# Optimization experiments

Measured on AMD Instinct MI355X. Metric: run time of the kernel, lower is better.

## Reference

```python
import jax, jax.numpy as jnp
import numpy as np

N_NODES = 100000
N_PART = 5000
N_EDGES = 1000000
D_NODE = 128
D_PART = 128
D_ATT = 20


def setup_inputs() -> dict:
    key = jax.random.key(0)
    ks = jax.random.split(key, 20)
    inp = {
        "nodes_hidden": jax.random.normal(ks[0], (N_NODES, D_NODE), jnp.float32),
        "particles_hidden": jax.random.normal(ks[1], (N_PART, D_PART), jnp.float32),
        "global_rep": jax.random.normal(ks[2], (N_PART, D_NODE), jnp.float32),
        "src": jax.random.randint(ks[3], (N_EDGES,), 0, N_NODES, jnp.int32),
        "dst": jax.random.randint(ks[4], (N_EDGES,), 0, N_PART, jnp.int32),
        "key_W": jax.random.normal(ks[5], (D_NODE, D_ATT), jnp.float32) * 0.05,
        "key_b": jnp.zeros((D_ATT,), jnp.float32),
        "val_W": jax.random.normal(ks[6], (D_NODE, D_PART), jnp.float32) * 0.05,
        "val_b": jnp.zeros((D_PART,), jnp.float32),
        "q_W": jax.random.normal(ks[7], (D_PART + D_NODE, D_ATT), jnp.float32) * 0.05,
        "q_b": jnp.zeros((D_ATT,), jnp.float32),
        "W_ih": jax.random.normal(ks[8], (3 * D_PART, D_PART), jnp.float32) * 0.05,
        "W_hh": jax.random.normal(ks[9], (3 * D_PART, D_PART), jnp.float32) * 0.05,
        "b_ih": jnp.zeros((3 * D_PART,), jnp.float32),
        "b_hh": jnp.zeros((3 * D_PART,), jnp.float32),
        "ln_g": jnp.ones((D_PART,), jnp.float32),
        "ln_b": jnp.zeros((D_PART,), jnp.float32),
        "mlp_W1": jax.random.normal(ks[10], (D_PART, 64), jnp.float32) * 0.05,
        "mlp_b1": jnp.zeros((64,), jnp.float32),
        "mlp_W2": jax.random.normal(ks[11], (64, D_PART), jnp.float32) * 0.05,
        "mlp_b2": jnp.zeros((D_PART,), jnp.float32),
    }
    return inp


def reference(nodes_hidden, particles_hidden, global_rep, src, dst,
              key_W, key_b, val_W, val_b, q_W, q_b,
              W_ih, W_hh, b_ih, b_hh, ln_g, ln_b,
              mlp_W1, mlp_b1, mlp_W2, mlp_b2):
    norm = jnp.float32(1.0) / jnp.sqrt(jnp.float32(D_ATT))
    keys = nodes_hidden @ key_W + key_b          # [N, 20]
    vals = nodes_hidden @ val_W + val_b          # [N, P]
    q_in = jnp.concatenate([particles_hidden, global_rep], axis=1)
    query = q_in @ q_W + q_b                     # [Np, 20]

    # per-edge raw attention (ReLU'd copy in edges.data is unused downstream)
    att = jnp.sum(keys[src] * query[dst], axis=1) * norm     # [E]
    msg = att[:, None] * vals[src]                            # [E, P]
    weighted_sum = jax.ops.segment_sum(msg, dst, num_segments=particles_hidden.shape[0])

    # GRUCell(input=weighted_sum, hidden=particles_hidden), torch semantics
    gi = weighted_sum @ W_ih.T + b_ih
    gh = particles_hidden @ W_hh.T + b_hh
    i_r, i_z, i_n = jnp.split(gi, 3, axis=1)
    h_r, h_z, h_n = jnp.split(gh, 3, axis=1)
    r = jax.nn.sigmoid(i_r + h_r)
    z = jax.nn.sigmoid(i_z + h_z)
    n = jnp.tanh(i_n + r * h_n)
    h_new = (1.0 - z) * n + z * particles_hidden

    # LayerNorm (eps=1e-5)
    mu = jnp.mean(h_new, axis=-1, keepdims=True)
    var = jnp.mean(jnp.square(h_new - mu), axis=-1, keepdims=True)
    ln = (h_new - mu) * jax.lax.rsqrt(var + 1e-5) * ln_g + ln_b

    mlp_out = jax.nn.relu(ln @ mlp_W1 + mlp_b1) @ mlp_W2 + mlp_b2
    return particles_hidden + mlp_out
```

## Files before the change

### kernel.cpp

```cpp
#include <hip/hip_runtime.h>
#include <math.h>

#define N_NODES 100000
#define N_PART  5000
#define N_EDGES 1000000
#define D_NODE  128
#define D_PART  128
#define D_ATT   20
#define NBLK    128
#define EPB     ((N_EDGES + NBLK - 1) / NBLK)
#define TPV6    8
#define QBLKS   (N_PART / TPV6)
#define CVTBLKS 1024

__device__ __forceinline__ float sigmoid_(float x) { return 1.f / (1.f + __expf(-x)); }
__device__ __forceinline__ float tanh_(float x)    { return 1.f - 2.f / (__expf(2.f * x) + 1.f); }

__device__ __forceinline__ float4 bf4_to_f4(uint2 r) {
    float4 f;
    f.x = __uint_as_float(r.x << 16);
    f.y = __uint_as_float(r.x & 0xFFFF0000u);
    f.z = __uint_as_float(r.y << 16);
    f.w = __uint_as_float(r.y & 0xFFFF0000u);
    return f;
}

__device__ __forceinline__ unsigned short f_to_bf(float v) {
    uint32_t u = __float_as_uint(v);
    return (unsigned short)((u + 0x7FFFu + ((u >> 16) & 1u)) >> 16);
}

__device__ __forceinline__ void gru_body(float4 acc[4],
    float4 w0, float4 w1, float4 w2, float4 w3,
    float4 x0, float4 x1, float4 x2, float4 x3)
{
    acc[0].x += x0.x * w0.x + x0.y * w1.x + x0.z * w2.x + x0.w * w3.x;
    acc[0].y += x0.x * w0.y + x0.y * w1.y + x0.z * w2.y + x0.w * w3.y;
    acc[0].z += x0.x * w0.z + x0.y * w1.z + x0.z * w2.z + x0.w * w3.z;
    acc[0].w += x0.x * w0.w + x0.y * w1.w + x0.z * w2.w + x0.w * w3.w;
    acc[1].x += x1.x * w0.x + x1.y * w1.x + x1.z * w2.x + x1.w * w3.x;
    acc[1].y += x1.x * w0.y + x1.y * w1.y + x1.z * w2.y + x1.w * w3.y;
    acc[1].z += x1.x * w0.z + x1.y * w1.z + x1.z * w2.z + x1.w * w3.z;
    acc[1].w += x1.x * w0.w + x1.y * w1.w + x1.z * w2.w + x1.w * w3.w;
    acc[2].x += x2.x * w0.x + x2.y * w1.x + x2.z * w2.x + x2.w * w3.x;
    acc[2].y += x2.x * w0.y + x2.y * w1.y + x2.z * w2.y + x2.w * w3.y;
    acc[2].z += x2.x * w0.z + x2.y * w1.z + x2.z * w2.z + x2.w * w3.z;
    acc[2].w += x2.x * w0.w + x2.y * w1.w + x2.z * w2.w + x2.w * w3.w;
    acc[3].x += x3.x * w0.x + x3.y * w1.x + x3.z * w2.x + x3.w * w3.x;
    acc[3].y += x3.x * w0.y + x3.y * w1.y + x3.z * w2.y + x3.w * w3.y;
    acc[3].z += x3.x * w0.z + x3.y * w1.z + x3.z * w2.z + x3.w * w3.z;
    acc[3].w += x3.x * w0.w + x3.y * w1.w + x3.z * w2.w + x3.w * w3.w;
}

__device__ __forceinline__ size_t wpk_idx(int k, int jn) {
    return ((size_t)(k >> 1) * 128 + (jn >> 2)) * 8 + ((k & 1) << 2) + (jn & 3);
}

__global__ __launch_bounds__(256) void fused_front_kernel(
    const float* __restrict__ valW, const float* __restrict__ Wih,
    const float* __restrict__ Whh, unsigned short* __restrict__ Wpack,
    const float* __restrict__ valb, float* __restrict__ bvec,
    const int* __restrict__ dst, int* __restrict__ blockhist,
    const float* __restrict__ ph, const float* __restrict__ gr,
    const float* __restrict__ qW, const float* __restrict__ qb,
    const float* __restrict__ keyW, const float* __restrict__ keyb,
    float* __restrict__ qk, float* __restrict__ qoff,
    const float* __restrict__ nodes, unsigned short* __restrict__ nodes_bf)
{
    __shared__ float pool[5000];
    int blk = blockIdx.x;
    int t = threadIdx.x;

    if (blk < 12) {
        float (*sA)[33] = (float (*)[33])pool;
        float (*sB)[33] = (float (*)[33])(pool + 2112);
        int bk = blk / 6, bj = blk - bk * 6;
        int k0 = bk * 64, j0 = bj * 64;
        int tk = t >> 4, tj = t & 15;
        float acc[4][4];
        #pragma unroll
        for (int i = 0; i < 4; i++)
            #pragma unroll
            for (int j = 0; j < 4; j++) acc[i][j] = 0.f;

        for (int mc = 0; mc < 128; mc += 32) {
            #pragma unroll
            for (int s = 0; s < 2; s++) {
                int f = t + s * 256;
                int r = f >> 3, c4 = (f & 7) * 4;
                *(float4*)&sA[r][c4] = *(const float4*)(valW + (size_t)(k0 + r) * 128 + mc + c4);
                *(float4*)&sB[r][c4] = *(const float4*)(Wih  + (size_t)(j0 + r) * 128 + mc + c4);
            }
            __syncthreads();
            #pragma unroll 8
            for (int mm = 0; mm < 32; mm++) {
                float a0 = sA[tk * 4 + 0][mm], a1 = sA[tk * 4 + 1][mm];
                float a2 = sA[tk * 4 + 2][mm], a3 = sA[tk * 4 + 3][mm];
                float b0 = sB[tj * 4 + 0][mm], b1 = sB[tj * 4 + 1][mm];
                float b2 = sB[tj * 4 + 2][mm], b3 = sB[tj * 4 + 3][mm];
                acc[0][0] += a0 * b0; acc[0][1] += a0 * b1; acc[0][2] += a0 * b2; acc[0][3] += a0 * b3;
                acc[1][0] += a1 * b0; acc[1][1] += a1 * b1; acc[1][2] += a1 * b2; acc[1][3] += a1 * b3;
                acc[2][0] += a2 * b0; acc[2][1] += a2 * b1; acc[2][2] += a2 * b2; acc[2][3] += a2 * b3;
                acc[3][0] += a3 * b0; acc[3][1] += a3 * b1; acc[3][2] += a3 * b2; acc[3][3] += a3 * b3;
            }
            __syncthreads();
        }
        #pragma unroll
        for (int i = 0; i < 4; i++) {
            int k = k0 + tk * 4 + i;
            #pragma unroll
            for (int j = 0; j < 4; j++) {
                int oj = j0 + tj * 4 + j;
                int jn = (oj & 127) * 4 + (oj >> 7);
                Wpack[wpk_idx(k, jn)] = f_to_bf(acc[i][j]);
            }
        }
    } else if (blk < 14) {
        for (int f = t; f < 8192; f += 256) {
            int e = (blk - 12) * 8192 + f;
            int k = e >> 7, c = e & 127;
            Wpack[wpk_idx(k, c * 4 + 3)] = 0;
        }
    } else if (blk < 142) {
        #pragma unroll
        for (int s = 0; s < 2; s++) {
            int idx = 65536 + (blk - 14) * 512 + s * 256 + t;
            int k = idx >> 9;
            int jn = idx & 511;
            int j = (jn & 3) * 128 + (jn >> 2);
            int kp = k - 128;
            float v = 0.f;
            if (j < 256)       v = Whh[j * 128 + kp];
            else if (j >= 384) v = Whh[(j - 128) * 128 + kp];
            Wpack[wpk_idx(k, jn)] = f_to_bf(v);
        }
    } else if (blk < 144) {
        int c = (blk - 142) * 256 + t;
        if (c < 384) {
            float acc = 0.f;
            #pragma unroll 8
            for (int m = 0; m < 128; m++) acc += valb[m] * Wih[c * 128 + m];
            bvec[c] = acc;
        }
    } else if (blk < 272) {
        int b = blk - 144;
        int* h = (int*)pool;
        for (int i = t; i < N_PART; i += 256) h[i] = 0;
        __syncthreads();
        int beg = b * EPB, end = min(beg + EPB, N_EDGES);
        for (int e = beg + t; e < end; e += 256)
            atomicAdd(&h[dst[e]], 1);
        __syncthreads();
        for (int i = t; i < N_PART; i += 256)
            blockhist[(size_t)b * N_PART + i] = h[i];
    } else if (blk < 897) {
        float (*s_in)[260] = (float (*)[260])pool;
        float (*s_q)[20]   = (float (*)[20])(pool + 2080);
        float (*s_kw)[21]  = (float (*)[21])(pool + 2240);
        float* s_kb = pool + 4928;
        float* s_qb = pool + 4948;

        int pbase = (blk - 272) * TPV6;

        for (int f = t; f < TPV6 * 64; f += 256) {
            int pl = f >> 6, r = f & 63;
            int c4 = r * 4;
            int p = pbase + pl;
            float4 v;
            if (c4 < 128) v = *(const float4*)(ph + (size_t)p * 128 + c4);
            else          v = *(const float4*)(gr + (size_t)p * 128 + (c4 - 128));
            *(float4*)&s_in[pl][c4] = v;
        }
        for (int f = t; f < 2560; f += 256) {
            int j = f / 20, a = f - j * 20;
            s_kw[j][a] = keyW[f];
        }
        if (t < 20) { s_kb[t] = keyb[t]; s_qb[t] = qb[t]; }
        __syncthreads();

        if (t < 160) {
            int pl = t / 20, a = t - (t / 20) * 20;
            float acc = s_qb[a];
            const float* qwp = qW + a;
            #pragma unroll 8
            for (int k = 0; k < 256; k++) acc += s_in[pl][k] * qwp[k * 20];
            s_q[pl][a] = acc;
        }
        __syncthreads();

        {
            int pl = t >> 5, j0 = (t & 31) * 4;
            float acc0 = 0.f, acc1 = 0.f, acc2 = 0.f, acc3 = 0.f;
            #pragma unroll
            for (int a = 0; a < 20; a++) {
                float qv = s_q[pl][a];
                acc0 += qv * s_kw[j0][a];
                acc1 += qv * s_kw[j0 + 1][a];
                acc2 += qv * s_kw[j0 + 2][a];
                acc3 += qv * s_kw[j0 + 3][a];
            }
            float4 o; o.x = acc0; o.y = acc1; o.z = acc2; o.w = acc3;
            *(float4*)(qk + (size_t)(pbase + pl) * 128 + j0) = o;

            if (t < TPV6) {
                float acc = 0.f;
                #pragma unroll
                for (int a = 0; a < 20; a++) acc += s_kb[a] * s_q[t][a];
                qoff[pbase + t] = acc;
            }
        }
    } else {
        const uint64_t total8 = (uint64_t)N_NODES * 128 / 8;
        uint64_t cb = (uint64_t)(blk - 897) * 256 + t;
        const uint32_t* inb = (const uint32_t*)nodes;
        uint32_t* outb = (uint32_t*)nodes_bf;
        for (uint64_t c = cb; c < total8; c += (uint64_t)CVTBLKS * 256) {
            uint4 a = *(const uint4*)(inb + c * 8);
            uint4 b = *(const uint4*)(inb + c * 8 + 4);
            uint32_t r0 = (a.x + 0x7FFFu + ((a.x >> 16) & 1u)) >> 16;
            uint32_t r1 = (a.y + 0x7FFFu + ((a.y >> 16) & 1u)) >> 16;
            uint32_t r2 = (a.z + 0x7FFFu + ((a.z >> 16) & 1u)) >> 16;
            uint32_t r3 = (a.w + 0x7FFFu + ((a.w >> 16) & 1u)) >> 16;
            uint32_t r4 = (b.x + 0x7FFFu + ((b.x >> 16) & 1u)) >> 16;
            uint32_t r5 = (b.y + 0x7FFFu + ((b.y >> 16) & 1u)) >> 16;
            uint32_t r6 = (b.z + 0x7FFFu + ((b.z >> 16) & 1u)) >> 16;
            uint32_t r7 = (b.w + 0x7FFFu + ((b.w >> 16) & 1u)) >> 16;
            uint4 o;
            o.x = r0 | (r1 << 16);
            o.y = r2 | (r3 << 16);
            o.z = r4 | (r5 << 16);
            o.w = r6 | (r7 << 16);
            *(uint4*)(outb + c * 4) = o;
        }
    }
}

__global__ __launch_bounds__(256) void colscan_kernel(
    int* __restrict__ blockhist, int* __restrict__ totals)
{
    int i = blockIdx.x * 256 + threadIdx.x;
    if (i >= N_PART) return;
    int run = 0;
    for (int b = 0; b < NBLK; b++) {
        size_t idx = (size_t)b * N_PART + i;
        int v = blockhist[idx];
        blockhist[idx] = run;
        run += v;
    }
    totals[i] = run;
}

__global__ __launch_bounds__(256) void scan_kernel(
    const int* __restrict__ totals, int* __restrict__ offsets)
{
    __shared__ int ss[256];
    int t = threadIdx.x;
    const int CH = 20;
    int beg = t * CH;
    int end = min(beg + CH, N_PART);
    int lsum = 0;
    for (int i = beg; i < end; i++) lsum += totals[i];
    ss[t] = lsum;
    __syncthreads();
    for (int off = 1; off < 256; off <<= 1) {
        int v = (t >= off) ? ss[t - off] : 0;
        __syncthreads();
        ss[t] += v;
        __syncthreads();
    }
    int base = ss[t] - lsum;
    for (int i = beg; i < end; i++) {
        offsets[i] = base;
        base += totals[i];
    }
    if (t == 0) offsets[N_PART] = N_EDGES;
}

__global__ __launch_bounds__(256) void scatter_sorted_kernel(
    const int* __restrict__ src, const int* __restrict__ dst,
    const int* __restrict__ offsets, const int* __restrict__ blockhist,
    int* __restrict__ ssrc)
{
    __shared__ int cur[N_PART];
    int b = blockIdx.x;
    for (int i = threadIdx.x; i < N_PART; i += 256)
        cur[i] = offsets[i] + blockhist[(size_t)b * N_PART + i];
    __syncthreads();
    int beg = b * EPB, end = min(beg + EPB, N_EDGES);
    for (int e = beg + threadIdx.x; e < end; e += 256) {
        int d = dst[e];
        int pos = atomicAdd(&cur[d], 1);
        ssrc[pos] = src[e];
    }
}

__global__ __launch_bounds__(256) void edge_agg_bf16_kernel(
    const unsigned short* __restrict__ nodes_bf, const float* __restrict__ qk,
    const float* __restrict__ qoff,
    const int* __restrict__ offsets, const int* __restrict__ ssrc,
    float* __restrict__ agg, float* __restrict__ att_sum)
{
    const float norm = 0.22360679774997896f;
    int p = blockIdx.x;
    int tid = threadIdx.x;
    int lane = tid & 63;
    int wave = tid >> 6;
    int half = lane >> 5;
    int colq = (lane & 31) * 4;

    const float4 q = *(const float4*)(qk + (size_t)p * 128 + colq);
    float qo = qoff[p];
    int beg = offsets[p], end = offsets[p + 1];
    int n = end - beg;
    int np = (n + 1) >> 1;
    int npfull = n >> 1;

    float4 a = {0.f, 0.f, 0.f, 0.f};
    float asum = 0.f;

    int pi = wave;
    for (; pi + 12 < npfull; pi += 16) {
        int e0 = beg + 2 * pi + half;
        int s0 = ssrc[e0];
        int s1 = ssrc[e0 + 8];
        int s2 = ssrc[e0 + 16];
        int s3 = ssrc[e0 + 24];
        uint2 r0 = *(const uint2*)(nodes_bf + (size_t)s0 * 128 + colq);
        uint2 r1 = *(const uint2*)(nodes_bf + (size_t)s1 * 128 + colq);
        uint2 r2 = *(const uint2*)(nodes_bf + (size_t)s2 * 128 + colq);
        uint2 r3 = *(const uint2*)(nodes_bf + (size_t)s3 * 128 + colq);
        float4 x0 = bf4_to_f4(r0);
        float4 x1 = bf4_to_f4(r1);
        float4 x2 = bf4_to_f4(r2);
        float4 x3 = bf4_to_f4(r3);
        float d0 = x0.x * q.x + x0.y * q.y + x0.z * q.z + x0.w * q.w;
        float d1 = x1.x * q.x + x1.y * q.y + x1.z * q.z + x1.w * q.w;
        float d2 = x2.x * q.x + x2.y * q.y + x2.z * q.z + x2.w * q.w;
        float d3 = x3.x * q.x + x3.y * q.y + x3.z * q.z + x3.w * q.w;
        #pragma unroll
        for (int off = 1; off <= 16; off <<= 1) {
            d0 += __shfl_xor(d0, off, 64);
            d1 += __shfl_xor(d1, off, 64);
            d2 += __shfl_xor(d2, off, 64);
            d3 += __shfl_xor(d3, off, 64);
        }
        float t0 = (d0 + qo) * norm;
        float t1 = (d1 + qo) * norm;
        float t2 = (d2 + qo) * norm;
        float t3 = (d3 + qo) * norm;
        a.x += t0 * x0.x + t1 * x1.x + t2 * x2.x + t3 * x3.x;
        a.y += t0 * x0.y + t1 * x1.y + t2 * x2.y + t3 * x3.y;
        a.z += t0 * x0.z + t1 * x1.z + t2 * x2.z + t3 * x3.z;
        a.w += t0 * x0.w + t1 * x1.w + t2 * x2.w + t3 * x3.w;
        asum += t0 + t1 + t2 + t3;
    }
    for (; pi < np; pi += 4) {
        int e0 = beg + 2 * pi;
        bool has1 = (e0 + 1 < end);
        int s0 = ssrc[e0];
        int s1 = has1 ? ssrc[e0 + 1] : s0;
        int s = half ? s1 : s0;
        uint2 r = *(const uint2*)(nodes_bf + (size_t)s * 128 + colq);
        float4 x = bf4_to_f4(r);
        float d = x.x * q.x + x.y * q.y + x.z * q.z + x.w * q.w;
        #pragma unroll
        for (int off = 1; off <= 16; off <<= 1) d += __shfl_xor(d, off, 64);
        float att = (d + qo) * norm;
        if (half && !has1) att = 0.f;
        a.x += att * x.x; a.y += att * x.y; a.z += att * x.z; a.w += att * x.w;
        asum += att;
    }

    a.x += __shfl_xor(a.x, 32, 64);
    a.y += __shfl_xor(a.y, 32, 64);
    a.z += __shfl_xor(a.z, 32, 64);
    a.w += __shfl_xor(a.w, 32, 64);
    asum += __shfl_xor(asum, 32, 64);

    __shared__ float s_acc[4][128];
    __shared__ float s_as[4];
    if (lane < 32) {
        *(float4*)&s_acc[wave][colq] = a;
        if (lane == 0) s_as[wave] = asum;
    }
    __syncthreads();

    if (tid < 128) {
        float v = s_acc[0][tid] + s_acc[1][tid] + s_acc[2][tid] + s_acc[3][tid];
        agg[(size_t)p * 128 + tid] = v;
        if (tid == 0) att_sum[p] = s_as[0] + s_as[1] + s_as[2] + s_as[3];
    }
}

__global__ __launch_bounds__(256) void gru_fused_v8(
    const float* __restrict__ agg, const float* __restrict__ att_sum,
    const float* __restrict__ ph,
    const unsigned short* __restrict__ Wpack, const float* __restrict__ bvec,
    const float* __restrict__ bih, const float* __restrict__ bhh,
    const float* __restrict__ lng, const float* __restrict__ lnb,
    const float* __restrict__ W1, const float* __restrict__ b1,
    const float* __restrict__ W2, const float* __restrict__ b2,
    float* __restrict__ out)
{
    __shared__ float s_in[TPV6][256];
    __shared__ float s_ln[TPV6][128];
    __shared__ float s_hid[TPV6][64];

    int t = threadIdx.x;
    int pbase = blockIdx.x * TPV6;

    for (int f = t; f < TPV6 * 64; f += 256) {
        int pl = f >> 6, r = f & 63;
        int c4 = r * 4;
        int p = pbase + pl;
        float4 v;
        if (c4 < 128) v = *(const float4*)(agg + (size_t)p * 128 + c4);
        else          v = *(const float4*)(ph + (size_t)p * 128 + (c4 - 128));
        *(float4*)&s_in[pl][c4] = v;
    }

    int c  = t & 127;
    int pg = t >> 7;
    float4 cb, bv;
    cb.x = bih[c]       + bhh[c];        bv.x = bvec[c];
    cb.y = bih[128 + c] + bhh[128 + c];  bv.y = bvec[128 + c];
    cb.z = bih[256 + c];                 bv.z = bvec[256 + c];
    cb.w = bhh[256 + c];                 bv.w = 0.f;
    float4 acc[4];
    #pragma unroll
    for (int i = 0; i < 4; i++) {
        float as = att_sum[pbase + pg * 4 + i];
        acc[i].x = cb.x + as * bv.x;
        acc[i].y = cb.y + as * bv.y;
        acc[i].z = cb.z + as * bv.z;
        acc[i].w = cb.w + as * bv.w;
    }
    __syncthreads();

    const uint4* wpk = (const uint4*)Wpack;
    uint4 wu = wpk[c];
    uint4 wv = wpk[128 + c];
    float4 x0 = *(const float4*)&s_in[pg * 4 + 0][0];
    float4 x1 = *(const float4*)&s_in[pg * 4 + 1][0];
    float4 x2 = *(const float4*)&s_in[pg * 4 + 2][0];
    float4 x3 = *(const float4*)&s_in[pg * 4 + 3][0];
    for (int k = 0; k < 256; k += 4) {
        uint4 cu = wu, cv = wv;
        float4 cx0 = x0, cx1 = x1, cx2 = x2, cx3 = x3;
        if (k < 252) {
            int k2n = (k >> 1) + 2;
            wu = wpk[(size_t)k2n * 128 + c];
            wv = wpk[(size_t)(k2n + 1) * 128 + c];
            x0 = *(const float4*)&s_in[pg * 4 + 0][k + 4];
            x1 = *(const float4*)&s_in[pg * 4 + 1][k + 4];
            x2 = *(const float4*)&s_in[pg * 4 + 2][k + 4];
            x3 = *(const float4*)&s_in[pg * 4 + 3][k + 4];
        }
        float4 w0 = bf4_to_f4(make_uint2(cu.x, cu.y));
        float4 w1 = bf4_to_f4(make_uint2(cu.z, cu.w));
        float4 w2 = bf4_to_f4(make_uint2(cv.x, cv.y));
        float4 w3 = bf4_to_f4(make_uint2(cv.z, cv.w));
        gru_body(acc, w0, w1, w2, w3, cx0, cx1, cx2, cx3);
    }

    #pragma unroll
    for (int i = 0; i < 4; i++) {
        int pl = pg * 4 + i;
        float r = sigmoid_(acc[i].x);
        float z = sigmoid_(acc[i].y);
        float n = tanh_(acc[i].z + r * acc[i].w);
        float h = s_in[pl][128 + c];
        s_ln[pl][c] = (1.f - z) * n + z * h;
    }
    __syncthreads();

    {
        int wv2 = t >> 6, l = t & 63;
        for (int pl = wv2; pl < TPV6; pl += 4) {
            float v0 = s_ln[pl][l * 2], v1 = s_ln[pl][l * 2 + 1];
            float sum = v0 + v1, sq = v0 * v0 + v1 * v1;
            #pragma unroll
            for (int off = 1; off <= 32; off <<= 1) {
                sum += __shfl_xor(sum, off, 64);
                sq  += __shfl_xor(sq, off, 64);
            }
            float mu = sum * (1.f / 128.f);
            float var = sq * (1.f / 128.f) - mu * mu;
            float rstd = rsqrtf(var + 1e-5f);
            s_ln[pl][l * 2]     = (v0 - mu) * rstd * lng[l * 2] + lnb[l * 2];
            s_ln[pl][l * 2 + 1] = (v1 - mu) * rstd * lng[l * 2 + 1] + lnb[l * 2 + 1];
        }
    }
    __syncthreads();

    for (int idx = t; idx < TPV6 * 64; idx += 256) {
        int pl = idx >> 6, u = idx & 63;
        float a0 = b1[u];
        #pragma unroll 4
        for (int k = 0; k < 128; k++) a0 += s_ln[pl][k] * W1[k * 64 + u];
        s_hid[pl][u] = fmaxf(a0, 0.f);
    }
    __syncthreads();

    for (int idx = t; idx < TPV6 * 32; idx += 256) {
        int pl = idx >> 5, qd = idx & 31;
        int c4 = qd * 4;
        float4 o = *(const float4*)(b2 + c4);
        #pragma unroll 4
        for (int u = 0; u < 64; u++) {
            float av = s_hid[pl][u];
            float4 w = *(const float4*)(W2 + u * 128 + c4);
            o.x += av * w.x; o.y += av * w.y; o.z += av * w.z; o.w += av * w.w;
        }
        float4 h4 = *(const float4*)&s_in[pl][128 + c4];
        float4 res;
        res.x = h4.x + o.x; res.y = h4.y + o.y;
        res.z = h4.z + o.z; res.w = h4.w + o.w;
        *(float4*)(out + (size_t)(pbase + pl) * 128 + c4) = res;
    }
}

extern "C" void kernel_launch(void* const* d_in, const int* in_sizes, int n_in,
                              void* d_out, int out_size, void* d_ws, size_t ws_size,
                              hipStream_t stream) {
    const float* nodes = (const float*)d_in[0];
    const float* ph    = (const float*)d_in[1];
    const float* gr    = (const float*)d_in[2];
    const int*   src   = (const int*)d_in[3];
    const int*   dst   = (const int*)d_in[4];
    const float* keyW  = (const float*)d_in[5];
    const float* keyb  = (const float*)d_in[6];
    const float* valW  = (const float*)d_in[7];
    const float* valb  = (const float*)d_in[8];
    const float* qW    = (const float*)d_in[9];
    const float* qb    = (const float*)d_in[10];
    const float* Wih   = (const float*)d_in[11];
    const float* Whh   = (const float*)d_in[12];
    const float* bih   = (const float*)d_in[13];
    const float* bhh   = (const float*)d_in[14];
    const float* lng   = (const float*)d_in[15];
    const float* lnb   = (const float*)d_in[16];
    const float* W1    = (const float*)d_in[17];
    const float* b1    = (const float*)d_in[18];
    const float* W2    = (const float*)d_in[19];
    const float* b2    = (const float*)d_in[20];
    float* out = (float*)d_out;

    float* ws_f      = (float*)d_ws;
    float* qk        = ws_f;
    float* qoff      = qk + 640000;
    float* agg       = qoff + 5008;
    float* att_sum   = agg + 640000;
    int*   totals    = (int*)(att_sum + 5008);
    int*   offsets   = totals + 5008;
    int*   blockhist = offsets + 5008;
    int*   ssrc      = blockhist + (size_t)NBLK * N_PART;
    unsigned short* Wpack = (unsigned short*)(ssrc + 1000000);
    float* bvec      = (float*)(Wpack + 131072);
    unsigned short* nodes_bf = (unsigned short*)(bvec + 512);

    fused_front_kernel<<<897 + CVTBLKS, 256, 0, stream>>>(
        valW, Wih, Whh, Wpack,
        valb, bvec,
        dst, blockhist,
        ph, gr, qW, qb, keyW, keyb, qk, qoff,
        nodes, nodes_bf);

    colscan_kernel<<<(N_PART + 255) / 256, 256, 0, stream>>>(blockhist, totals);

    scan_kernel<<<1, 256, 0, stream>>>(totals, offsets);

    scatter_sorted_kernel<<<NBLK, 256, 0, stream>>>(src, dst, offsets, blockhist, ssrc);

    edge_agg_bf16_kernel<<<N_PART, 256, 0, stream>>>(nodes_bf, qk, qoff, offsets, ssrc, agg, att_sum);

    gru_fused_v8<<<N_PART / TPV6, 256, 0, stream>>>(
        agg, att_sum, ph, Wpack, bvec, bih, bhh, lng, lnb, W1, b1, W2, b2, out);
}
```

Measured before the change: 269.3 us.

## Use fp32 packed GRU weights and halve particles per block in GRU kernel

The combined GRU weight matrix is now stored as plain fp32 in a simple row-major [k][512] layout instead of a bf16 pair-interleaved pack, so the GRU kernel loads float4s directly with no conversion. The GRU kernel also processes 4 particles per block instead of 8, which doubles the grid to 1250 blocks and halves per-thread accumulators. The goal is more parallelism and less register pressure in this tail kernel. In exchange, weight traffic per block doubles in bytes and the total weight reads across blocks grow, and precision of the GRU weights goes up slightly.

```diff
diff --git a/kernel.cpp b/kernel.cpp
--- a/kernel.cpp
+++ b/kernel.cpp
@@ -11,6 +11,7 @@
 #define EPB     ((N_EDGES + NBLK - 1) / NBLK)
 #define TPV6    8
 #define QBLKS   (N_PART / TPV6)
+#define TPV9    4
 #define CVTBLKS 1024
 
 __device__ __forceinline__ float sigmoid_(float x) { return 1.f / (1.f + __expf(-x)); }
@@ -25,14 +26,9 @@
     return f;
 }
 
-__device__ __forceinline__ unsigned short f_to_bf(float v) {
-    uint32_t u = __float_as_uint(v);
-    return (unsigned short)((u + 0x7FFFu + ((u >> 16) & 1u)) >> 16);
-}
-
-__device__ __forceinline__ void gru_body(float4 acc[4],
+__device__ __forceinline__ void gru_body2(float4 acc[2],
     float4 w0, float4 w1, float4 w2, float4 w3,
-    float4 x0, float4 x1, float4 x2, float4 x3)
+    float4 x0, float4 x1)
 {
     acc[0].x += x0.x * w0.x + x0.y * w1.x + x0.z * w2.x + x0.w * w3.x;
     acc[0].y += x0.x * w0.y + x0.y * w1.y + x0.z * w2.y + x0.w * w3.y;
@@ -42,23 +38,11 @@
     acc[1].y += x1.x * w0.y + x1.y * w1.y + x1.z * w2.y + x1.w * w3.y;
     acc[1].z += x1.x * w0.z + x1.y * w1.z + x1.z * w2.z + x1.w * w3.z;
     acc[1].w += x1.x * w0.w + x1.y * w1.w + x1.z * w2.w + x1.w * w3.w;
-    acc[2].x += x2.x * w0.x + x2.y * w1.x + x2.z * w2.x + x2.w * w3.x;
-    acc[2].y += x2.x * w0.y + x2.y * w1.y + x2.z * w2.y + x2.w * w3.y;
-    acc[2].z += x2.x * w0.z + x2.y * w1.z + x2.z * w2.z + x2.w * w3.z;
-    acc[2].w += x2.x * w0.w + x2.y * w1.w + x2.z * w2.w + x2.w * w3.w;
-    acc[3].x += x3.x * w0.x + x3.y * w1.x + x3.z * w2.x + x3.w * w3.x;
-    acc[3].y += x3.x * w0.y + x3.y * w1.y + x3.z * w2.y + x3.w * w3.y;
-    acc[3].z += x3.x * w0.z + x3.y * w1.z + x3.z * w2.z + x3.w * w3.z;
-    acc[3].w += x3.x * w0.w + x3.y * w1.w + x3.z * w2.w + x3.w * w3.w;
-}
-
-__device__ __forceinline__ size_t wpk_idx(int k, int jn) {
-    return ((size_t)(k >> 1) * 128 + (jn >> 2)) * 8 + ((k & 1) << 2) + (jn & 3);
 }
 
 __global__ __launch_bounds__(256) void fused_front_kernel(
     const float* __restrict__ valW, const float* __restrict__ Wih,
-    const float* __restrict__ Whh, unsigned short* __restrict__ Wpack,
+    const float* __restrict__ Whh, float* __restrict__ Wbig,
     const float* __restrict__ valb, float* __restrict__ bvec,
     const int* __restrict__ dst, int* __restrict__ blockhist,
     const float* __restrict__ ph, const float* __restrict__ gr,
@@ -111,15 +95,14 @@
             #pragma unroll
             for (int j = 0; j < 4; j++) {
                 int oj = j0 + tj * 4 + j;
-                int jn = (oj & 127) * 4 + (oj >> 7);
-                Wpack[wpk_idx(k, jn)] = f_to_bf(acc[i][j]);
+                Wbig[(size_t)k * 512 + (oj & 127) * 4 + (oj >> 7)] = acc[i][j];
             }
         }
     } else if (blk < 14) {
         for (int f = t; f < 8192; f += 256) {
             int e = (blk - 12) * 8192 + f;
             int k = e >> 7, c = e & 127;
-            Wpack[wpk_idx(k, c * 4 + 3)] = 0;
+            Wbig[(size_t)k * 512 + c * 4 + 3] = 0.f;
         }
     } else if (blk < 142) {
         #pragma unroll
@@ -132,7 +115,7 @@
             float v = 0.f;
             if (j < 256)       v = Whh[j * 128 + kp];
             else if (j >= 384) v = Whh[(j - 128) * 128 + kp];
-            Wpack[wpk_idx(k, jn)] = f_to_bf(v);
+            Wbig[(size_t)k * 512 + jn] = v;
         }
     } else if (blk < 144) {
         int c = (blk - 142) * 256 + t;
@@ -392,24 +375,25 @@
     }
 }
 
-__global__ __launch_bounds__(256) void gru_fused_v8(
+__global__ __launch_bounds__(256) void gru_fused_v9(
     const float* __restrict__ agg, const float* __restrict__ att_sum,
     const float* __restrict__ ph,
-    const unsigned short* __restrict__ Wpack, const float* __restrict__ bvec,
+    const float* __restrict__ Wbig, const float* __restrict__ bvec,
     const float* __restrict__ bih, const float* __restrict__ bhh,
     const float* __restrict__ lng, const float* __restrict__ lnb,
     const float* __restrict__ W1, const float* __restrict__ b1,
     const float* __restrict__ W2, const float* __restrict__ b2,
     float* __restrict__ out)
 {
-    __shared__ float s_in[TPV6][256];
-    __shared__ float s_ln[TPV6][128];
-    __shared__ float s_hid[TPV6][64];
+    __shared__ float s_in[TPV9][256];
+    __shared__ float s_ln[TPV9][128];
+    __shared__ float s_hid[TPV9][64];
 
     int t = threadIdx.x;
-    int pbase = blockIdx.x * TPV6;
-
-    for (int f = t; f < TPV6 * 64; f += 256) {
+    int pbase = blockIdx.x * TPV9;
+
+    {
+        int f = t;
         int pl = f >> 6, r = f & 63;
         int c4 = r * 4;
         int p = pbase + pl;
@@ -420,16 +404,17 @@
     }
 
     int c  = t & 127;
+    int j4 = c * 4;
     int pg = t >> 7;
     float4 cb, bv;
     cb.x = bih[c]       + bhh[c];        bv.x = bvec[c];
     cb.y = bih[128 + c] + bhh[128 + c];  bv.y = bvec[128 + c];
     cb.z = bih[256 + c];                 bv.z = bvec[256 + c];
     cb.w = bhh[256 + c];                 bv.w = 0.f;
-    float4 acc[4];
+    float4 acc[2];
     #pragma unroll
-    for (int i = 0; i < 4; i++) {
-        float as = att_sum[pbase + pg * 4 + i];
+    for (int i = 0; i < 2; i++) {
+        float as = att_sum[pbase + pg * 2 + i];
         acc[i].x = cb.x + as * bv.x;
         acc[i].y = cb.y + as * bv.y;
         acc[i].z = cb.z + as * bv.z;
@@ -437,35 +422,31 @@
     }
     __syncthreads();
 
-    const uint4* wpk = (const uint4*)Wpack;
-    uint4 wu = wpk[c];
-    uint4 wv = wpk[128 + c];
-    float4 x0 = *(const float4*)&s_in[pg * 4 + 0][0];
-    float4 x1 = *(const float4*)&s_in[pg * 4 + 1][0];
-    float4 x2 = *(const float4*)&s_in[pg * 4 + 2][0];
-    float4 x3 = *(const float4*)&s_in[pg * 4 + 3][0];
+    const float* wp = Wbig + j4;
+    float4 w0 = *(const float4*)(wp);
+    float4 w1 = *(const float4*)(wp + 512);
+    float4 w2 = *(const float4*)(wp + 1024);
+    float4 w3 = *(const float4*)(wp + 1536);
+    float4 x0 = *(const float4*)&s_in[pg * 2 + 0][0];
+    float4 x1 = *(const float4*)&s_in[pg * 2 + 1][0];
     for (int k = 0; k < 256; k += 4) {
-        uint4 cu = wu, cv = wv;
-        float4 cx0 = x0, cx1 = x1, cx2 = x2, cx3 = x3;
+        float4 cw0 = w0, cw1 = w1, cw2 = w2, cw3 = w3;
+        float4 cx0 = x0, cx1 = x1;
         if (k < 252) {
-            int k2n = (k >> 1) + 2;
-            wu = wpk[(size_t)k2n * 128 + c];
-            wv = wpk[(size_t)(k2n + 1) * 128 + c];
-            x0 = *(const float4*)&s_in[pg * 4 + 0][k + 4];
-            x1 = *(const float4*)&s_in[pg * 4 + 1][k + 4];
-            x2 = *(const float4*)&s_in[pg * 4 + 2][k + 4];
-            x3 = *(const float4*)&s_in[pg * 4 + 3][k + 4];
-        }
-        float4 w0 = bf4_to_f4(make_uint2(cu.x, cu.y));
-        float4 w1 = bf4_to_f4(make_uint2(cu.z, cu.w));
-        float4 w2 = bf4_to_f4(make_uint2(cv.x, cv.y));
-        float4 w3 = bf4_to_f4(make_uint2(cv.z, cv.w));
-        gru_body(acc, w0, w1, w2, w3, cx0, cx1, cx2, cx3);
+            const float* wn = wp + (size_t)(k + 4) * 512;
+            w0 = *(const float4*)(wn);
+            w1 = *(const float4*)(wn + 512);
+            w2 = *(const float4*)(wn + 1024);
+            w3 = *(const float4*)(wn + 1536);
+            x0 = *(const float4*)&s_in[pg * 2 + 0][k + 4];
+            x1 = *(const float4*)&s_in[pg * 2 + 1][k + 4];
+        }
+        gru_body2(acc, cw0, cw1, cw2, cw3, cx0, cx1);
     }
 
     #pragma unroll
-    for (int i = 0; i < 4; i++) {
-        int pl = pg * 4 + i;
+    for (int i = 0; i < 2; i++) {
+        int pl = pg * 2 + i;
         float r = sigmoid_(acc[i].x);
         float z = sigmoid_(acc[i].y);
         float n = tanh_(acc[i].z + r * acc[i].w);
@@ -475,26 +456,25 @@
     __syncthreads();
 
     {
-        int wv2 = t >> 6, l = t & 63;
-        for (int pl = wv2; pl < TPV6; pl += 4) {
-            float v0 = s_ln[pl][l * 2], v1 = s_ln[pl][l * 2 + 1];
-            float sum = v0 + v1, sq = v0 * v0 + v1 * v1;
-            #pragma unroll
-            for (int off = 1; off <= 32; off <<= 1) {
-                sum += __shfl_xor(sum, off, 64);
-                sq  += __shfl_xor(sq, off, 64);
-            }
-            float mu = sum * (1.f / 128.f);
-            float var = sq * (1.f / 128.f) - mu * mu;
-            float rstd = rsqrtf(var + 1e-5f);
-            s_ln[pl][l * 2]     = (v0 - mu) * rstd * lng[l * 2] + lnb[l * 2];
-            s_ln[pl][l * 2 + 1] = (v1 - mu) * rstd * lng[l * 2 + 1] + lnb[l * 2 + 1];
-        }
-    }
-    __syncthreads();
-
-    for (int idx = t; idx < TPV6 * 64; idx += 256) {
-        int pl = idx >> 6, u = idx & 63;
+        int wv = t >> 6, l = t & 63;
+        int pl = wv;
+        float v0 = s_ln[pl][l * 2], v1 = s_ln[pl][l * 2 + 1];
+        float sum = v0 + v1, sq = v0 * v0 + v1 * v1;
+        #pragma unroll
+        for (int off = 1; off <= 32; off <<= 1) {
+            sum += __shfl_xor(sum, off, 64);
+            sq  += __shfl_xor(sq, off, 64);
+        }
+        float mu = sum * (1.f / 128.f);
+        float var = sq * (1.f / 128.f) - mu * mu;
+        float rstd = rsqrtf(var + 1e-5f);
+        s_ln[pl][l * 2]     = (v0 - mu) * rstd * lng[l * 2] + lnb[l * 2];
+        s_ln[pl][l * 2 + 1] = (v1 - mu) * rstd * lng[l * 2 + 1] + lnb[l * 2 + 1];
+    }
+    __syncthreads();
+
+    {
+        int pl = t >> 6, u = t & 63;
         float a0 = b1[u];
         #pragma unroll 4
         for (int k = 0; k < 128; k++) a0 += s_ln[pl][k] * W1[k * 64 + u];
@@ -502,8 +482,8 @@
     }
     __syncthreads();
 
-    for (int idx = t; idx < TPV6 * 32; idx += 256) {
-        int pl = idx >> 5, qd = idx & 31;
+    if (t < TPV9 * 32) {
+        int pl = t >> 5, qd = t & 31;
         int c4 = qd * 4;
         float4 o = *(const float4*)(b2 + c4);
         #pragma unroll 4
@@ -555,12 +535,12 @@
     int*   offsets   = totals + 5008;
     int*   blockhist = offsets + 5008;
     int*   ssrc      = blockhist + (size_t)NBLK * N_PART;
-    unsigned short* Wpack = (unsigned short*)(ssrc + 1000000);
-    float* bvec      = (float*)(Wpack + 131072);
+    float* Wbig      = (float*)(ssrc + 1000000);
+    float* bvec      = Wbig + 131072;
     unsigned short* nodes_bf = (unsigned short*)(bvec + 512);
 
     fused_front_kernel<<<897 + CVTBLKS, 256, 0, stream>>>(
-        valW, Wih, Whh, Wpack,
+        valW, Wih, Whh, Wbig,
         valb, bvec,
         dst, blockhist,
         ph, gr, qW, qb, keyW, keyb, qk, qoff,
@@ -574,6 +554,6 @@
 
     edge_agg_bf16_kernel<<<N_PART, 256, 0, stream>>>(nodes_bf, qk, qoff, offsets, ssrc, agg, att_sum);
 
-    gru_fused_v8<<<N_PART / TPV6, 256, 0, stream>>>(
-        agg, att_sum, ph, Wpack, bvec, bih, bhh, lng, lnb, W1, b1, W2, b2, out);
-}
+    gru_fused_v9<<<N_PART / TPV9, 256, 0, stream>>>(
+        agg, att_sum, ph, Wbig, bvec, bih, bhh, lng, lnb, W1, b1, W2, b2, out);
+}
```

Result: slower. 280.7 us (+4.2%).
